# Kernel tuning notes

Hardware: AMD Instinct MI355X
Metric: run time of the kernel (lower is better)

## Reference

```python
import jax, jax.numpy as jnp
import numpy as np

N, D, H, O, E = 50000, 512, 512, 256, 150000
NEG_SLOPE = 0.2
EPS = 1e-16


def gat_conv(x, edge_index, W_src, W_dst, a_src, a_dst, bias):
    """Single-head PyG GATConv, add_self_loops=False.
    x: [N, Din]; edge_index: [2, E] (row 0 = src, row 1 = dst).
    W_src/W_dst: [Din, C]; a_src/a_dst: [C]; bias: [C].
    """
    src, dst = edge_index[0], edge_index[1]
    h_src = x @ W_src                      # [N, C]
    h_dst = x @ W_dst                      # [N, C]
    alpha_src = h_src @ a_src              # [N]
    alpha_dst = h_dst @ a_dst              # [N]
    e = jax.nn.leaky_relu(alpha_src[src] + alpha_dst[dst], NEG_SLOPE)  # [E]
    # per-destination segment softmax (numerically stable)
    m = jax.ops.segment_max(e, dst, num_segments=N)       # [N]
    ex = jnp.exp(e - m[dst])                               # [E]
    s = jax.ops.segment_sum(ex, dst, num_segments=N)       # [N]
    alpha = ex / (s[dst] + EPS)                            # [E]
    # scatter-add weighted source messages to destinations
    out = jax.ops.segment_sum(alpha[:, None] * h_src[src], dst, num_segments=N)  # [N, C]
    return out + bias


def setup_inputs() -> dict:
    key = jax.random.key(0)
    ks = jax.random.split(key, 20)
    g = lambda i, shape, sc: (jax.random.normal(ks[i], shape, dtype=jnp.float32) * sc)
    inp = {
        "x": jax.random.normal(ks[0], (N, D), dtype=jnp.float32),
        "edge_index": jax.random.randint(ks[1], (2, E), 0, N, dtype=jnp.int32),
        "edge_index_2_hop": jax.random.randint(ks[2], (2, E), 0, N, dtype=jnp.int32),
        # conv1 (D -> H)
        "W1_src": g(3, (D, H), 0.05), "W1_dst": g(4, (D, H), 0.05),
        "a1_src": g(5, (H,), 0.05), "a1_dst": g(6, (H,), 0.05),
        "b1": jnp.zeros((H,), jnp.float32),
        # lin1 (H -> H)
        "Wl1": g(7, (H, H), 0.05), "bl1": jnp.zeros((H,), jnp.float32),
        # conv2 (H -> O)
        "W2_src": g(8, (H, O), 0.05), "W2_dst": g(9, (H, O), 0.05),
        "a2_src": g(10, (O,), 0.05), "a2_dst": g(11, (O,), 0.05),
        "b2": jnp.zeros((O,), jnp.float32),
        # lin2 (O -> O)
        "Wl2": g(12, (O, O), 0.05), "bl2": jnp.zeros((O,), jnp.float32),
    }
    return inp


def reference(x, edge_index, edge_index_2_hop,
              W1_src, W1_dst, a1_src, a1_dst, b1, Wl1, bl1,
              W2_src, W2_dst, a2_src, a2_dst, b2, Wl2, bl2):
    h = (gat_conv(x, edge_index, W1_src, W1_dst, a1_src, a1_dst, b1)
         + gat_conv(x, edge_index_2_hop, W1_src, W1_dst, a1_src, a1_dst, b1))
    h = jax.nn.relu(h @ Wl1 + bl1)
    h = (gat_conv(h, edge_index, W2_src, W2_dst, a2_src, a2_dst, b2)
         + gat_conv(h, edge_index_2_hop, W2_src, W2_dst, a2_src, a2_dst, b2))
    return h @ Wl2 + bl2
```

## Files before the change

kernel.cpp:

```cpp
#include <hip/hip_runtime.h>

typedef unsigned short u16;
typedef __attribute__((ext_vector_type(8))) unsigned short v8u16;
typedef __attribute__((ext_vector_type(4))) unsigned short v4u16;
typedef __attribute__((ext_vector_type(8))) __bf16 v8bf;
typedef __attribute__((ext_vector_type(4))) float v4f;

#define NN 50000
#define EE 150000
#define SCAN_CHUNK 512
#define NB_PER_SET 98

__device__ inline float b2f(u16 u) {
    union { unsigned int i; float f; } x; x.i = ((unsigned int)u) << 16; return x.f;
}
__device__ inline u16 f2b(float f) {
    union { float f; unsigned int i; } x; x.f = f;
    unsigned int r = x.i + 0x7FFFu + ((x.i >> 16) & 1u);
    return (u16)(r >> 16);
}
__device__ inline float wred(float v) {
    v += __shfl_down(v, 32, 64);
    v += __shfl_down(v, 16, 64);
    v += __shfl_down(v, 8, 64);
    v += __shfl_down(v, 4, 64);
    v += __shfl_down(v, 2, 64);
    v += __shfl_down(v, 1, 64);
    return v;
}
__device__ inline int wred_i(int v) {
    v += __shfl_down(v, 32, 64);
    v += __shfl_down(v, 16, 64);
    v += __shfl_down(v, 8, 64);
    v += __shfl_down(v, 4, 64);
    v += __shfl_down(v, 2, 64);
    v += __shfl_down(v, 1, 64);
    return v;
}

__device__ __forceinline__ void gll16(const u16* g, u16* l) {
    __builtin_amdgcn_global_load_lds(
        (const __attribute__((address_space(1))) void*)g,
        (__attribute__((address_space(3))) void*)l, 16, 0, 0);
}


__global__ void transpose4(const float* __restrict__ W0, u16* __restrict__ T0,
                           const float* __restrict__ W1, u16* __restrict__ T1,
                           const float* __restrict__ W2, u16* __restrict__ T2,
                           const float* __restrict__ W3, u16* __restrict__ T3) {
    int idx = blockIdx.x * blockDim.x + threadIdx.x;
    const float* W; u16* T; int N, K, base;
    if (idx < 262144)      { W = W0; T = T0; K = 512; N = 512; base = 0; }
    else if (idx < 524288) { W = W1; T = T1; K = 512; N = 512; base = 262144; }
    else if (idx < 655360) { W = W2; T = T2; K = 512; N = 256; base = 524288; }
    else if (idx < 720896) { W = W3; T = T3; K = 256; N = 256; base = 655360; }
    else return;
    int i = idx - base;
    int n = i % N, k = i / N;
    T[(size_t)n * K + k] = f2b(W[i]);
}

__global__ void wv4(const float* __restrict__ Wa, const float* __restrict__ Wb,
                    const float* __restrict__ Wc, const float* __restrict__ Wd,
                    const float* __restrict__ aa, const float* __restrict__ ab,
                    const float* __restrict__ ac, const float* __restrict__ ad,
                    float* __restrict__ vbuf) {
    int rw = (blockIdx.x * blockDim.x + threadIdx.x) >> 6;
    int lane = threadIdx.x & 63;
    if (rw >= 2048) return;
    int seg = rw >> 9, r = rw & 511;
    const float* W; const float* a; int C;
    if (seg == 0)      { W = Wa; a = aa; C = 512; }
    else if (seg == 1) { W = Wb; a = ab; C = 512; }
    else if (seg == 2) { W = Wc; a = ac; C = 256; }
    else               { W = Wd; a = ad; C = 256; }
    float s = 0.f;
    int c0 = lane * 8;
    if (c0 < C) {
        const float* wp = W + (size_t)r * C + c0;
        v4f w0 = *(const v4f*)wp;
        v4f w1 = *(const v4f*)(wp + 4);
        v4f a0 = *(const v4f*)(a + c0);
        v4f a1 = *(const v4f*)(a + c0 + 4);
#pragma unroll
        for (int j = 0; j < 4; ++j) s += w0[j] * a0[j] + w1[j] * a1[j];
    }
    s = wred(s);
    if (lane == 0) vbuf[rw] = s;
}

__global__ void alpha_pair_f32x(const float* __restrict__ X, const float* __restrict__ vs,
                                const float* __restrict__ vd, float* __restrict__ as_,
                                float* __restrict__ ad_, u16* __restrict__ Xb, int Nn) {
    int w = (blockIdx.x * blockDim.x + threadIdx.x) >> 6;
    int lane = threadIdx.x & 63;
    if (w >= Nn) return;
    const float* xp = X + (size_t)w * 512 + lane * 8;
    v4f x0 = *(const v4f*)xp;
    v4f x1 = *(const v4f*)(xp + 4);
    const float* vsp = vs + lane * 8;
    const float* vdp = vd + lane * 8;
    float s1 = 0.f, s2 = 0.f;
    v8u16 o;
#pragma unroll
    for (int j = 0; j < 4; ++j) {
        s1 += x0[j] * vsp[j] + x1[j] * vsp[j + 4];
        s2 += x0[j] * vdp[j] + x1[j] * vdp[j + 4];
        o[j] = f2b(x0[j]); o[j + 4] = f2b(x1[j]);
    }
    *(v8u16*)(Xb + (size_t)w * 512 + lane * 8) = o;
    s1 = wred(s1);
    s2 = wred(s2);
    if (lane == 0) { as_[w] = s1; ad_[w] = s2; }
}

__global__ void alpha_pair_bf16(const u16* __restrict__ X, const float* __restrict__ vs,
                                const float* __restrict__ vd, float* __restrict__ as_,
                                float* __restrict__ ad_, int Nn) {
    int w = (blockIdx.x * blockDim.x + threadIdx.x) >> 6;
    int lane = threadIdx.x & 63;
    if (w >= Nn) return;
    v8u16 xv = *(const v8u16*)(X + (size_t)w * 512 + lane * 8);
    const float* vsp = vs + lane * 8;
    const float* vdp = vd + lane * 8;
    float s1 = 0.f, s2 = 0.f;
#pragma unroll
    for (int j = 0; j < 8; ++j) {
        float xf = b2f(xv[j]);
        s1 += xf * vsp[j];
        s2 += xf * vdp[j];
    }
    s1 = wred(s1);
    s2 = wred(s2);
    if (lane == 0) { as_[w] = s1; ad_[w] = s2; }
}


__global__ void deg2_kernel(const int* __restrict__ ei1, const int* __restrict__ ei2,
                            int* __restrict__ deg) {
    int idx = blockIdx.x * blockDim.x + threadIdx.x;
    if (idx >= 2 * EE) return;
    int set = idx >= EE;
    int e = idx - set * EE;
    const int* ei = set ? ei2 : ei1;
    atomicAdd(&deg[set * NN + ei[EE + e]], 1);
}

__global__ void scan_partial(const int* __restrict__ deg, int* __restrict__ bsum) {
    int b = blockIdx.x;
    int set = b / NB_PER_SET, lb = b - set * NB_PER_SET;
    int tid = threadIdx.x;
    int i0 = lb * SCAN_CHUNK + tid * 2;
    int s = 0;
    if (i0 < NN)     s += deg[set * NN + i0];
    if (i0 + 1 < NN) s += deg[set * NN + i0 + 1];
    s = wred_i(s);
    __shared__ int lsum[4];
    if ((tid & 63) == 0) lsum[tid >> 6] = s;
    __syncthreads();
    if (tid == 0) bsum[b] = lsum[0] + lsum[1] + lsum[2] + lsum[3];
}

__global__ void scan_tops(int* __restrict__ bsum) {
    __shared__ int ls[256];
    int tid = threadIdx.x;
    int set = tid >> 7, lb = tid & 127;
    int v = (lb < NB_PER_SET) ? bsum[set * NB_PER_SET + lb] : 0;
    ls[tid] = v;
    __syncthreads();
    for (int off = 1; off < 128; off <<= 1) {
        int t = (lb >= off) ? ls[tid - off] : 0;
        __syncthreads();
        ls[tid] += t;
        __syncthreads();
    }
    if (lb < NB_PER_SET) bsum[set * NB_PER_SET + lb] = ls[tid] - v;
}

__global__ void scan_final(const int* __restrict__ deg, const int* __restrict__ bsum,
                           int* __restrict__ rp) {
    int b = blockIdx.x;
    int set = b / NB_PER_SET, lb = b - set * NB_PER_SET;
    int tid = threadIdx.x;
    int i0 = lb * SCAN_CHUNK + tid * 2;
    int d0 = (i0 < NN)     ? deg[set * NN + i0]     : 0;
    int d1 = (i0 + 1 < NN) ? deg[set * NN + i0 + 1] : 0;
    int pair = d0 + d1;
    __shared__ int ps[256];
    ps[tid] = pair;
    __syncthreads();
    for (int off = 1; off < 256; off <<= 1) {
        int t = (tid >= off) ? ps[tid - off] : 0;
        __syncthreads();
        ps[tid] += t;
        __syncthreads();
    }
    int base = bsum[b] + ps[tid] - pair;
    if (i0 < NN)     rp[set * (NN + 1) + i0] = base;
    if (i0 + 1 < NN) rp[set * (NN + 1) + i0 + 1] = base + d0;
    if (b == 0 && tid == 0) { rp[NN] = EE; rp[(NN + 1) + NN] = EE; }
}

__global__ void fill2_kernel(const int* __restrict__ ei1, const int* __restrict__ ei2,
                             const int* __restrict__ rp, int* __restrict__ deg,
                             int* __restrict__ srcp, int* __restrict__ dstp) {
    int idx = blockIdx.x * blockDim.x + threadIdx.x;
    if (idx >= 2 * EE) return;
    int set = idx >= EE;
    int e = idx - set * EE;
    const int* ei = set ? ei2 : ei1;
    int d = ei[EE + e];
    int old = atomicSub(&deg[set * NN + d], 1);
    int pos = rp[set * (NN + 1) + d] + old - 1;
    srcp[set * EE + pos] = ei[e];
    dstp[set * EE + pos] = d;
}

__global__ void edge_ex(const int* __restrict__ srcp, const int* __restrict__ dstp,
                        const float* __restrict__ asrc, const float* __restrict__ adst,
                        float* __restrict__ ex) {
    int i = blockIdx.x * blockDim.x + threadIdx.x;
    if (i >= 2 * EE) return;
    float t = asrc[srcp[i]] + adst[dstp[i]];
    t = t > 0.f ? t : 0.2f * t;
    ex[i] = __expf(fminf(t, 60.f));
}

template <int CV>
__global__ void gat_pull(const int* __restrict__ rp, const int* __restrict__ srcp,
                         const float* __restrict__ ex, const u16* __restrict__ H,
                         const float* __restrict__ bias, u16* __restrict__ G, int Nn) {
    const int C = CV * 64;
    int d = (blockIdx.x * blockDim.x + threadIdx.x) >> 6;
    int lane = threadIdx.x & 63;
    if (d >= Nn) return;
    float out[CV];
#pragma unroll
    for (int j = 0; j < CV; ++j) out[j] = 0.f;
#pragma unroll
    for (int set = 0; set < 2; ++set) {
        const int* rpS = rp + set * (NN + 1);
        int base = set * EE;
        int beg = rpS[d], end = rpS[d + 1];
        float acc[CV];
#pragma unroll
        for (int j = 0; j < CV; ++j) acc[j] = 0.f;
        float ssum = 0.f;
        for (int i = beg; i < end; ++i) {
            float w = ex[base + i];
            int s = srcp[base + i];
            ssum += w;
            const u16* hp = H + (size_t)s * C + lane * CV;
            if constexpr (CV == 8) {
                v8u16 hv = *(const v8u16*)hp;
#pragma unroll
                for (int j = 0; j < 8; ++j) acc[j] += w * b2f(hv[j]);
            } else {
                v4u16 hv = *(const v4u16*)hp;
#pragma unroll
                for (int j = 0; j < 4; ++j) acc[j] += w * b2f(hv[j]);
            }
        }
        float inv = 1.f / (ssum + 1e-16f);
#pragma unroll
        for (int j = 0; j < CV; ++j) out[j] += acc[j] * inv;
    }
    const float* bp = bias + lane * CV;
    u16* gp = G + (size_t)d * C + lane * CV;
    if constexpr (CV == 8) {
        v8u16 o;
#pragma unroll
        for (int j = 0; j < 8; ++j) o[j] = f2b(out[j] + 2.f * bp[j]);
        *(v8u16*)gp = o;
    } else {
        v4u16 o;
#pragma unroll
        for (int j = 0; j < 4; ++j) o[j] = f2b(out[j] + 2.f * bp[j]);
        *(v4u16*)gp = o;
    }
}

__global__ __launch_bounds__(256, 2) void gemm_bf16(
    const u16* __restrict__ A, const u16* __restrict__ Bt, void* __restrict__ Cv,
    int M, int N, int K, const float* __restrict__ bias, int relu, int outf32) {
    __shared__ u16 As[128 * 32];
    __shared__ u16 Bs[128 * 32];
    const int tid = threadIdx.x;
    const int lane = tid & 63;
    const int wid = tid >> 6;
    const int wm = wid >> 1;
    const int wn = wid & 1;
    const int quad = lane >> 4;
    const int l16 = lane & 15;
    const int tileM = blockIdx.y * 128;
    const int tileN = blockIdx.x * 128;

    const int srow = tid >> 2;
    const int scol = (tid & 3) * 8;
    int ra0 = tileM + srow;       if (ra0 >= M) ra0 = M - 1;
    int ra1 = tileM + 64 + srow;  if (ra1 >= M) ra1 = M - 1;
    const u16* gA0 = A + (size_t)ra0 * K + scol;
    const u16* gA1 = A + (size_t)ra1 * K + scol;
    const u16* gB0 = Bt + (size_t)(tileN + srow) * K + scol;
    const u16* gB1 = Bt + (size_t)(tileN + 64 + srow) * K + scol;
    u16* lA0 = As + wid * 512;
    u16* lA1 = As + 2048 + wid * 512;
    u16* lB0 = Bs + wid * 512;
    u16* lB1 = Bs + 2048 + wid * 512;

    v4f acc[4][4];
#pragma unroll
    for (int i = 0; i < 4; ++i)
#pragma unroll
        for (int j = 0; j < 4; ++j) acc[i][j] = v4f{0.f, 0.f, 0.f, 0.f};

    for (int k0 = 0; k0 < K; k0 += 32) {
        gll16(gA0 + k0, lA0);
        gll16(gA1 + k0, lA1);
        gll16(gB0 + k0, lB0);
        gll16(gB1 + k0, lB1);
        __syncthreads();
        v8bf af[4], bfr[4];
#pragma unroll
        for (int i = 0; i < 4; ++i)
            af[i] = __builtin_bit_cast(v8bf, *(const v8u16*)&As[(wm * 64 + i * 16 + l16) * 32 + quad * 8]);
#pragma unroll
        for (int i = 0; i < 4; ++i)
            bfr[i] = __builtin_bit_cast(v8bf, *(const v8u16*)&Bs[(wn * 64 + i * 16 + l16) * 32 + quad * 8]);
#pragma unroll
        for (int mi = 0; mi < 4; ++mi)
#pragma unroll
            for (int ni = 0; ni < 4; ++ni)
                acc[mi][ni] = __builtin_amdgcn_mfma_f32_16x16x32_bf16(af[mi], bfr[ni], acc[mi][ni], 0, 0, 0);
        __syncthreads();
    }

#pragma unroll
    for (int mi = 0; mi < 4; ++mi)
#pragma unroll
        for (int ni = 0; ni < 4; ++ni) {
            int col = tileN + wn * 64 + ni * 16 + l16;
            float bb = bias ? bias[col] : 0.f;
            int row0 = tileM + wm * 64 + mi * 16 + quad * 4;
#pragma unroll
            for (int r = 0; r < 4; ++r) {
                int row = row0 + r;
                if (row < M) {
                    float v = acc[mi][ni][r] + bb;
                    if (relu) v = fmaxf(v, 0.f);
                    if (outf32) ((float*)Cv)[(size_t)row * N + col] = v;
                    else        ((u16*)Cv)[(size_t)row * N + col] = f2b(v);
                }
            }
        }
}


extern "C" void kernel_launch(void* const* d_in, const int* in_sizes, int n_in,
                              void* d_out, int out_size, void* d_ws, size_t ws_size,
                              hipStream_t stream) {
    const float* x  = (const float*)d_in[0];
    const int* ei1  = (const int*)d_in[1];
    const int* ei2  = (const int*)d_in[2];
    const float* W1s = (const float*)d_in[3];
    const float* W1d = (const float*)d_in[4];
    const float* a1s = (const float*)d_in[5];
    const float* a1d = (const float*)d_in[6];
    const float* b1  = (const float*)d_in[7];
    const float* Wl1 = (const float*)d_in[8];
    const float* bl1 = (const float*)d_in[9];
    const float* W2s = (const float*)d_in[10];
    const float* W2d = (const float*)d_in[11];
    const float* a2s = (const float*)d_in[12];
    const float* a2d = (const float*)d_in[13];
    const float* b2  = (const float*)d_in[14];
    const float* Wl2 = (const float*)d_in[15];
    const float* bl2 = (const float*)d_in[16];
    float* out = (float*)d_out;

    char* ws = (char*)d_ws;
    size_t off = 0;
    auto alloc = [&](size_t b) { void* p = ws + off; off = (off + b + 255) & ~(size_t)255; return p; };
    u16* bufA   = (u16*)alloc((size_t)NN * 512 * 2);
    u16* bufB   = (u16*)alloc((size_t)NN * 512 * 2);
    int* rp     = (int*)alloc((size_t)2 * (NN + 1) * 4);
    int* srcp   = (int*)alloc((size_t)2 * EE * 4);
    int* dstp   = (int*)alloc((size_t)2 * EE * 4);
    int* deg    = (int*)alloc((size_t)2 * NN * 4);
    int* bsum   = (int*)alloc((size_t)2 * NB_PER_SET * 4);
    float* ex   = (float*)alloc((size_t)2 * EE * 4);
    float* asrc = (float*)alloc((size_t)NN * 4);
    float* adst = (float*)alloc((size_t)NN * 4);
    float* vbuf = (float*)alloc(2048 * 4);
    u16* Wt1s   = (u16*)alloc((size_t)512 * 512 * 2);
    u16* Wtl1   = (u16*)alloc((size_t)512 * 512 * 2);
    u16* Wt2s   = (u16*)alloc((size_t)512 * 256 * 2);
    u16* Wtl2   = (u16*)alloc((size_t)256 * 256 * 2);
    u16* g2buf  = bufB + (size_t)NN * 256;

    hipMemsetAsync(deg, 0, (size_t)2 * NN * 4, stream);
    deg2_kernel<<<(2 * EE + 255) / 256, 256, 0, stream>>>(ei1, ei2, deg);
    scan_partial<<<2 * NB_PER_SET, 256, 0, stream>>>(deg, bsum);
    scan_tops<<<1, 256, 0, stream>>>(bsum);
    scan_final<<<2 * NB_PER_SET, 256, 0, stream>>>(deg, bsum, rp);
    fill2_kernel<<<(2 * EE + 255) / 256, 256, 0, stream>>>(ei1, ei2, rp, deg, srcp, dstp);

    transpose4<<<(720896 + 255) / 256, 256, 0, stream>>>(W1s, Wt1s, Wl1, Wtl1, W2s, Wt2s, Wl2, Wtl2);
    wv4<<<512, 256, 0, stream>>>(W1s, W1d, W2s, W2d, a1s, a1d, a2s, a2d, vbuf);

    alpha_pair_f32x<<<(NN + 3) / 4, 256, 0, stream>>>(x, vbuf, vbuf + 512, asrc, adst, bufB, NN);
    edge_ex<<<(2 * EE + 255) / 256, 256, 0, stream>>>(srcp, dstp, asrc, adst, ex);
    gemm_bf16<<<dim3(4, 391), 256, 0, stream>>>(bufB, Wt1s, bufA, NN, 512, 512, nullptr, 0, 0);
    gat_pull<8><<<(NN + 3) / 4, 256, 0, stream>>>(rp, srcp, ex, bufA, b1, bufB, NN);
    gemm_bf16<<<dim3(4, 391), 256, 0, stream>>>(bufB, Wtl1, bufA, NN, 512, 512, bl1, 1, 0);

    alpha_pair_bf16<<<(NN + 3) / 4, 256, 0, stream>>>(bufA, vbuf + 1024, vbuf + 1536, asrc, adst, NN);
    edge_ex<<<(2 * EE + 255) / 256, 256, 0, stream>>>(srcp, dstp, asrc, adst, ex);
    gemm_bf16<<<dim3(2, 391), 256, 0, stream>>>(bufA, Wt2s, bufB, NN, 256, 512, nullptr, 0, 0);
    gat_pull<4><<<(NN + 3) / 4, 256, 0, stream>>>(rp, srcp, ex, bufB, b2, g2buf, NN);
    gemm_bf16<<<dim3(2, 391), 256, 0, stream>>>(g2buf, Wtl2, out, NN, 256, 256, bl2, 0, 1);

    (void)in_sizes; (void)n_in; (void)out_size; (void)ws_size;
}
```

Before: 537.9 us.

## Double-buffer GEMM LDS, remap blocks per XCD, fuse alpha dots into epilogue

```diff
diff --git a/kernel.cpp b/kernel.cpp
--- a/kernel.cpp
+++ b/kernel.cpp
@@ -115,27 +115,6 @@
     if (lane == 0) { as_[w] = s1; ad_[w] = s2; }
 }
 
-__global__ void alpha_pair_bf16(const u16* __restrict__ X, const float* __restrict__ vs,
-                                const float* __restrict__ vd, float* __restrict__ as_,
-                                float* __restrict__ ad_, int Nn) {
-    int w = (blockIdx.x * blockDim.x + threadIdx.x) >> 6;
-    int lane = threadIdx.x & 63;
-    if (w >= Nn) return;
-    v8u16 xv = *(const v8u16*)(X + (size_t)w * 512 + lane * 8);
-    const float* vsp = vs + lane * 8;
-    const float* vdp = vd + lane * 8;
-    float s1 = 0.f, s2 = 0.f;
-#pragma unroll
-    for (int j = 0; j < 8; ++j) {
-        float xf = b2f(xv[j]);
-        s1 += xf * vsp[j];
-        s2 += xf * vdp[j];
-    }
-    s1 = wred(s1);
-    s2 = wred(s2);
-    if (lane == 0) { as_[w] = s1; ad_[w] = s2; }
-}
-
 
 __global__ void deg2_kernel(const int* __restrict__ ei1, const int* __restrict__ ei2,
                             int* __restrict__ deg) {
@@ -283,9 +262,11 @@
 
 __global__ __launch_bounds__(256, 2) void gemm_bf16(
     const u16* __restrict__ A, const u16* __restrict__ Bt, void* __restrict__ Cv,
-    int M, int N, int K, const float* __restrict__ bias, int relu, int outf32) {
-    __shared__ u16 As[128 * 32];
-    __shared__ u16 Bs[128 * 32];
+    int M, int N, int K, const float* __restrict__ bias, int relu, int outf32,
+    const float* __restrict__ avs, const float* __restrict__ avd,
+    float* __restrict__ aout_s, float* __restrict__ aout_d) {
+    __shared__ u16 As[2][128 * 32];
+    __shared__ u16 Bs[2][128 * 32];
     const int tid = threadIdx.x;
     const int lane = tid & 63;
     const int wid = tid >> 6;
@@ -293,8 +274,14 @@
     const int wn = wid & 1;
     const int quad = lane >> 4;
     const int l16 = lane & 15;
-    const int tileM = blockIdx.y * 128;
-    const int tileN = blockIdx.x * 128;
+
+    const int nwg = gridDim.x * gridDim.y;
+    const int orig = blockIdx.y * gridDim.x + blockIdx.x;
+    const int q = nwg >> 3, r = nwg & 7;
+    const int xcd = orig & 7, loc = orig >> 3;
+    const int wg = (xcd < r ? xcd * (q + 1) : r * (q + 1) + (xcd - r) * q) + loc;
+    const int tileM = (wg / gridDim.x) * 128;
+    const int tileN = (wg % gridDim.x) * 128;
 
     const int srow = tid >> 2;
     const int scol = (tid & 3) * 8;
@@ -304,10 +291,6 @@
     const u16* gA1 = A + (size_t)ra1 * K + scol;
     const u16* gB0 = Bt + (size_t)(tileN + srow) * K + scol;
     const u16* gB1 = Bt + (size_t)(tileN + 64 + srow) * K + scol;
-    u16* lA0 = As + wid * 512;
-    u16* lA1 = As + 2048 + wid * 512;
-    u16* lB0 = Bs + wid * 512;
-    u16* lB1 = Bs + 2048 + wid * 512;
 
     v4f acc[4][4];
 #pragma unroll
@@ -315,26 +298,43 @@
 #pragma unroll
         for (int j = 0; j < 4; ++j) acc[i][j] = v4f{0.f, 0.f, 0.f, 0.f};
 
-    for (int k0 = 0; k0 < K; k0 += 32) {
-        gll16(gA0 + k0, lA0);
-        gll16(gA1 + k0, lA1);
-        gll16(gB0 + k0, lB0);
-        gll16(gB1 + k0, lB1);
-        __syncthreads();
+    const int nt = K >> 5;
+    gll16(gA0, &As[0][wid * 512]);
+    gll16(gA1, &As[0][2048 + wid * 512]);
+    gll16(gB0, &Bs[0][wid * 512]);
+    gll16(gB1, &Bs[0][2048 + wid * 512]);
+    __syncthreads();
+
+    int cur = 0;
+    for (int t = 0; t < nt; ++t) {
+        if (t + 1 < nt) {
+            int kk = (t + 1) << 5;
+            gll16(gA0 + kk, &As[cur ^ 1][wid * 512]);
+            gll16(gA1 + kk, &As[cur ^ 1][2048 + wid * 512]);
+            gll16(gB0 + kk, &Bs[cur ^ 1][wid * 512]);
+            gll16(gB1 + kk, &Bs[cur ^ 1][2048 + wid * 512]);
+        }
         v8bf af[4], bfr[4];
 #pragma unroll
         for (int i = 0; i < 4; ++i)
-            af[i] = __builtin_bit_cast(v8bf, *(const v8u16*)&As[(wm * 64 + i * 16 + l16) * 32 + quad * 8]);
+            af[i] = __builtin_bit_cast(v8bf, *(const v8u16*)&As[cur][(wm * 64 + i * 16 + l16) * 32 + quad * 8]);
 #pragma unroll
         for (int i = 0; i < 4; ++i)
-            bfr[i] = __builtin_bit_cast(v8bf, *(const v8u16*)&Bs[(wn * 64 + i * 16 + l16) * 32 + quad * 8]);
+            bfr[i] = __builtin_bit_cast(v8bf, *(const v8u16*)&Bs[cur][(wn * 64 + i * 16 + l16) * 32 + quad * 8]);
 #pragma unroll
         for (int mi = 0; mi < 4; ++mi)
 #pragma unroll
             for (int ni = 0; ni < 4; ++ni)
                 acc[mi][ni] = __builtin_amdgcn_mfma_f32_16x16x32_bf16(af[mi], bfr[ni], acc[mi][ni], 0, 0, 0);
         __syncthreads();
-    }
+        cur ^= 1;
+    }
+
+    float rs[4][4], rd[4][4];
+#pragma unroll
+    for (int mi = 0; mi < 4; ++mi)
+#pragma unroll
+        for (int rr = 0; rr < 4; ++rr) { rs[mi][rr] = 0.f; rd[mi][rr] = 0.f; }
 
 #pragma unroll
     for (int mi = 0; mi < 4; ++mi)
@@ -342,18 +342,40 @@
         for (int ni = 0; ni < 4; ++ni) {
             int col = tileN + wn * 64 + ni * 16 + l16;
             float bb = bias ? bias[col] : 0.f;
+            float ws_ = avs ? avs[col] : 0.f;
+            float wd_ = avd ? avd[col] : 0.f;
             int row0 = tileM + wm * 64 + mi * 16 + quad * 4;
 #pragma unroll
-            for (int r = 0; r < 4; ++r) {
-                int row = row0 + r;
+            for (int rr = 0; rr < 4; ++rr) {
+                int row = row0 + rr;
                 if (row < M) {
-                    float v = acc[mi][ni][r] + bb;
+                    float v = acc[mi][ni][rr] + bb;
                     if (relu) v = fmaxf(v, 0.f);
                     if (outf32) ((float*)Cv)[(size_t)row * N + col] = v;
                     else        ((u16*)Cv)[(size_t)row * N + col] = f2b(v);
+                    rs[mi][rr] += v * ws_;
+                    rd[mi][rr] += v * wd_;
                 }
             }
         }
+
+    if (avs) {
+#pragma unroll
+        for (int mi = 0; mi < 4; ++mi)
+#pragma unroll
+            for (int rr = 0; rr < 4; ++rr) {
+                int row = tileM + wm * 64 + mi * 16 + quad * 4 + rr;
+                float a = rs[mi][rr], b = rd[mi][rr];
+                a += __shfl_down(a, 8, 64); a += __shfl_down(a, 4, 64);
+                a += __shfl_down(a, 2, 64); a += __shfl_down(a, 1, 64);
+                b += __shfl_down(b, 8, 64); b += __shfl_down(b, 4, 64);
+                b += __shfl_down(b, 2, 64); b += __shfl_down(b, 1, 64);
+                if (l16 == 0 && row < M) {
+                    atomicAdd(&aout_s[row], a);
+                    atomicAdd(&aout_d[row], b);
+                }
+            }
+    }
 }
 
 
@@ -411,15 +433,20 @@
 
     alpha_pair_f32x<<<(NN + 3) / 4, 256, 0, stream>>>(x, vbuf, vbuf + 512, asrc, adst, bufB, NN);
     edge_ex<<<(2 * EE + 255) / 256, 256, 0, stream>>>(srcp, dstp, asrc, adst, ex);
-    gemm_bf16<<<dim3(4, 391), 256, 0, stream>>>(bufB, Wt1s, bufA, NN, 512, 512, nullptr, 0, 0);
+    gemm_bf16<<<dim3(4, 391), 256, 0, stream>>>(bufB, Wt1s, bufA, NN, 512, 512, nullptr, 0, 0,
+                                                nullptr, nullptr, nullptr, nullptr);
     gat_pull<8><<<(NN + 3) / 4, 256, 0, stream>>>(rp, srcp, ex, bufA, b1, bufB, NN);
-    gemm_bf16<<<dim3(4, 391), 256, 0, stream>>>(bufB, Wtl1, bufA, NN, 512, 512, bl1, 1, 0);
-
-    alpha_pair_bf16<<<(NN + 3) / 4, 256, 0, stream>>>(bufA, vbuf + 1024, vbuf + 1536, asrc, adst, NN);
+    hipMemsetAsync(asrc, 0, (size_t)NN * 4, stream);
+    hipMemsetAsync(adst, 0, (size_t)NN * 4, stream);
+    gemm_bf16<<<dim3(4, 391), 256, 0, stream>>>(bufB, Wtl1, bufA, NN, 512, 512, bl1, 1, 0,
+                                                vbuf + 1024, vbuf + 1536, asrc, adst);
+
     edge_ex<<<(2 * EE + 255) / 256, 256, 0, stream>>>(srcp, dstp, asrc, adst, ex);
-    gemm_bf16<<<dim3(2, 391), 256, 0, stream>>>(bufA, Wt2s, bufB, NN, 256, 512, nullptr, 0, 0);
+    gemm_bf16<<<dim3(2, 391), 256, 0, stream>>>(bufA, Wt2s, bufB, NN, 256, 512, nullptr, 0, 0,
+                                                nullptr, nullptr, nullptr, nullptr);
     gat_pull<4><<<(NN + 3) / 4, 256, 0, stream>>>(rp, srcp, ex, bufB, b2, g2buf, NN);
-    gemm_bf16<<<dim3(2, 391), 256, 0, stream>>>(g2buf, Wtl2, out, NN, 256, 256, bl2, 0, 1);
+    gemm_bf16<<<dim3(2, 391), 256, 0, stream>>>(g2buf, Wtl2, out, NN, 256, 256, bl2, 0, 1,
+                                                nullptr, nullptr, nullptr, nullptr);
 
     (void)in_sizes; (void)n_in; (void)out_size; (void)ws_size;
 }
```

New measurement: 524.6 us. 2.5% less time.
